# Performance work log

Measured on AMD Instinct MI355X. Metric: run time of the kernel, lower is better.

## Reference

```python
import jax, jax.numpy as jnp
import numpy as np

B, N, D, EPG = 64, 1024, 128, 8192          # graphs, nodes/graph, feat dim, edges/graph
NTOT, ETOT = B * N, B * EPG
RATIO, LAMB, NEG = 0.8, 1.0, 0.2
K = int(np.ceil(RATIO * N))                  # 820 kept nodes per graph (static)


def setup_inputs() -> dict:
    key = jax.random.key(0)
    k1, k2, k3, k4, k5, k6 = jax.random.split(key, 6)
    feat = jax.random.normal(k1, (NTOT, D), jnp.float32)
    offs = (jnp.arange(B, dtype=jnp.int32) * N)[:, None]
    src = (jax.random.randint(k2, (B, EPG), 0, N, jnp.int32) + offs).reshape(-1)
    dst = (jax.random.randint(k3, (B, EPG), 0, N, jnp.int32) + offs).reshape(-1)
    e_feat = jnp.ones((ETOT,), jnp.float32)  # default e_feat=None -> ones
    # xavier-normal-ish params
    W = jax.random.normal(k4, (D, D), jnp.float32) * (2.0 / (D + D)) ** 0.5
    a = jax.random.normal(k5, (D, 1), jnp.float32) * (2.0 / (D + 1)) ** 0.5
    att = jax.random.normal(k6, (1, 2 * D), jnp.float32) * (2.0 / (1 + 2 * D)) ** 0.5
    return {"feat": feat, "e_feat": e_feat, "W": W, "a": a, "att": att,
            "src": src, "dst": dst}


def sparsemax(z, axis):
    """Dense sparsemax along `axis` (shift-invariant, same as edge_sparsemax
    per destination-node group after max subtraction)."""
    n = z.shape[axis]
    zs = -jnp.sort(-z, axis=axis)                      # descending
    cs = jnp.cumsum(zs, axis=axis)
    shp = [1] * z.ndim
    shp[axis] = n
    r = jnp.arange(1, n + 1, dtype=z.dtype).reshape(shp)
    supp = (1.0 + r * zs) > cs
    kz = supp.sum(axis=axis, keepdims=True)            # support size
    tau = (jnp.take_along_axis(cs, kz - 1, axis=axis) - 1.0) / kz.astype(z.dtype)
    return jnp.clip(z - tau, 0.0)


def reference(feat, e_feat, W, a, att, src, dst):
    # ---- NodeInfoScoreLayer (sym_norm=True) ----
    ones_e = jnp.ones_like(e_feat)
    out_deg = jax.ops.segment_sum(ones_e, src, NTOT)   # degrees incl. self loops
    in_deg = jax.ops.segment_sum(ones_e, dst, NTOT)
    sn = jnp.maximum(out_deg, 1.0) ** -0.5
    dn = jnp.maximum(in_deg, 1.0) ** -0.5
    nonself = (src != dst).astype(feat.dtype)          # remove_self_loop
    msg = (feat * sn[:, None])[src] * (e_feat * nonself)[:, None]   # u_mul_e
    agg = jax.ops.segment_sum(msg, dst, NTOT)                        # sum -> h
    info = jnp.abs(feat - agg * dn[:, None]).sum(axis=1)

    # ---- node attention gate ----
    attn = jax.nn.sigmoid(jax.nn.leaky_relu((feat @ W) @ a, 0.2).squeeze(-1))
    x_score = info * attn

    # ---- per-graph top-k (equal graph sizes -> static k) ----
    _, idx = jax.lax.top_k(x_score.reshape(B, N), K)
    perm = (idx + jnp.arange(B, dtype=idx.dtype)[:, None] * N).reshape(-1)
    feat_p = feat[perm]                                # [B*K, D]

    # ---- structure learning, sample=False path: per-graph dense blocks ----
    maskarr = jnp.full((NTOT,), -1, jnp.int32).at[perm].set(
        jnp.arange(B * K, dtype=jnp.int32))
    nr, nc = maskarr[src], maskarr[dst]
    valid = (nr >= 0) & (nc >= 0)                      # edges of pooled subgraph
    nr0 = jnp.where(valid, nr, 0)
    nc0 = jnp.where(valid, nc, 0)
    bb, ii, jj = nr0 // K, nr0 % K, nc0 % K            # block-diagonal coords

    fp = feat_p.reshape(B, K, D)
    wsrc = fp @ att[0, :D]                             # [B, K]
    wdst = fp @ att[0, D:]
    Wblk = jax.nn.leaky_relu(wsrc[:, :, None] + wdst[:, None, :], NEG)  # [B,K,K]
    Wblk = Wblk.at[bb, ii, jj].add(jnp.where(valid, LAMB * e_feat, 0.0))

    # edge_sparsemax: normalize over incoming edges of each dst node
    weights = sparsemax(Wblk, axis=1)                  # over src axis
    weights = jnp.where(jnp.abs(weights) > 1e-9, weights, 0.0)

    return feat_p, weights, perm, x_score
```

## Files before the change

### kernel.cpp

```cpp
#include <hip/hip_runtime.h>
#include <math.h>


static constexpr int B_    = 64;
static constexpr int N_    = 1024;
static constexpr int D_    = 128;
static constexpr int NTOT_ = B_ * N_;
static constexpr int ETOT_ = B_ * 8192;
static constexpr int K_    = 820;
static constexpr int BK_   = B_ * K_;
static constexpr float NEG_ = 0.2f;
static constexpr int CH_   = 128;
static constexpr int CPB_  = 7;
static constexpr int CAP_  = 64;

__device__ __forceinline__ float lrelu(float x) { return x >= 0.f ? x : NEG_ * x; }

__global__ void k_wa(const float* __restrict__ W, const float* __restrict__ a,
                     float* __restrict__ waf) {
  int d = threadIdx.x;
  double s = 0.0;
  for (int k = 0; k < D_; ++k) s += (double)W[d * D_ + k] * (double)a[k];
  waf[d] = (float)s;
}

__global__ void k_deg(const int* __restrict__ src, const int* __restrict__ dst,
                      int* __restrict__ outd, int* __restrict__ ind) {
  int e = blockIdx.x * 256 + threadIdx.x;
  atomicAdd(&outd[src[e]], 1);
  atomicAdd(&ind[dst[e]], 1);
}

__global__ void k_scansum(const int* __restrict__ in, int n, int* __restrict__ bsum) {
  int blk = blockIdx.x, t = threadIdx.x;
  int base = blk * 1024 + t * 4;
  int s = 0;
#pragma unroll
  for (int q = 0; q < 4; ++q) { int i = base + q; if (i < n) s += in[i]; }
#pragma unroll
  for (int off = 32; off > 0; off >>= 1) s += __shfl_down(s, off);
  __shared__ int ws[4];
  int w = t >> 6, lane = t & 63;
  if (lane == 0) ws[w] = s;
  __syncthreads();
  if (t == 0) bsum[blk] = ws[0] + ws[1] + ws[2] + ws[3];
}

__global__ void k_scanout(const int* __restrict__ in, int n,
                          const int* __restrict__ bsum, int* __restrict__ out) {
  int blk = blockIdx.x, t = threadIdx.x;
  int w = t >> 6, lane = t & 63;
  __shared__ int sbase;
  __shared__ int wtot[4];
  if (w == 0) {
    int v = (lane < blk) ? bsum[lane] : 0;
#pragma unroll
    for (int off = 32; off > 0; off >>= 1) v += __shfl_down(v, off);
    if (lane == 0) sbase = v;
  }
  int base = blk * 1024 + t * 4;
  int a0 = (base < n) ? in[base] : 0;
  int a1 = (base + 1 < n) ? in[base + 1] : 0;
  int a2 = (base + 2 < n) ? in[base + 2] : 0;
  int a3 = (base + 3 < n) ? in[base + 3] : 0;
  int s = a0 + a1 + a2 + a3;
  int inc = s;
#pragma unroll
  for (int off = 1; off < 64; off <<= 1) {
    int vv = __shfl_up(inc, off);
    if (lane >= off) inc += vv;
  }
  if (lane == 63) wtot[w] = inc;
  __syncthreads();
  int wbase = 0;
  for (int q = 0; q < w; ++q) wbase += wtot[q];
  int ex = sbase + wbase + inc - s;
  if (base < n) out[base] = ex; ex += a0;
  if (base + 1 < n) out[base + 1] = ex; ex += a1;
  if (base + 2 < n) out[base + 2] = ex; ex += a2;
  if (base + 3 < n) out[base + 3] = ex; ex += a3;
  if (blk == (int)gridDim.x - 1 && t == 255) out[n] = ex;
}

__global__ void k_fillcsr(const int* __restrict__ dst, const int* __restrict__ rowptr,
                          int* __restrict__ cursor, int* __restrict__ col) {
  int e = blockIdx.x * 256 + threadIdx.x;
  int v = dst[e];
  int p = atomicAdd(&cursor[v], 1);
  col[rowptr[v] + p] = e;
}

__global__ void k_agg(const float* __restrict__ feat, const float* __restrict__ e_feat,
                      const int* __restrict__ src, const int* __restrict__ col,
                      const int* __restrict__ rowptr, const int* __restrict__ outd,
                      const int* __restrict__ ind, const float* __restrict__ waf,
                      float* __restrict__ out_xs) {
  __shared__ int su[4][CAP_];
  __shared__ float ssc[4][CAP_];
  int g = blockIdx.x;
  int vb = (g & 7) * 2048 + (g >> 3);
  int w = threadIdx.x >> 6, lane = threadIdx.x & 63;
  int v = vb * 4 + w;
  int r0 = rowptr[v], r1 = rowptr[v + 1];
  int m = r1 - r0;
  int mm = m < CAP_ ? m : CAP_;
  for (int s = lane; s < mm; s += 64) {
    int e = col[r0 + s];
    int u = src[e];
    float sc = (u == v) ? 0.f : e_feat[e] / sqrtf(fmaxf((float)outd[u], 1.f));
    su[w][s] = u;
    ssc[w][s] = sc;
  }
  __syncthreads();
  const float2* f2 = (const float2*)feat;
  float2 f = f2[(size_t)v * 64 + lane];
  float ax = 0.f, ay = 0.f;
  int s = 0;
  for (; s + 4 <= mm; s += 4) {
    int u0 = su[w][s], u1 = su[w][s + 1], u2 = su[w][s + 2], u3 = su[w][s + 3];
    float c0 = ssc[w][s], c1 = ssc[w][s + 1], c2 = ssc[w][s + 2], c3 = ssc[w][s + 3];
    float2 f0 = f2[(size_t)u0 * 64 + lane];
    float2 f1 = f2[(size_t)u1 * 64 + lane];
    float2 fq = f2[(size_t)u2 * 64 + lane];
    float2 f3 = f2[(size_t)u3 * 64 + lane];
    ax += f0.x * c0 + f1.x * c1 + fq.x * c2 + f3.x * c3;
    ay += f0.y * c0 + f1.y * c1 + fq.y * c2 + f3.y * c3;
  }
  for (; s < mm; ++s) {
    float2 fu = f2[(size_t)su[w][s] * 64 + lane];
    ax += fu.x * ssc[w][s];
    ay += fu.y * ssc[w][s];
  }
  for (int sP = r0 + CAP_; sP < r1; ++sP) {
    int e = col[sP];
    int u = src[e];
    if (u == v) continue;
    float sc = e_feat[e] / sqrtf(fmaxf((float)outd[u], 1.f));
    float2 fu = f2[(size_t)u * 64 + lane];
    ax += fu.x * sc;
    ay += fu.y * sc;
  }
  float dn = 1.f / sqrtf(fmaxf((float)ind[v], 1.f));
  float info = fabsf(f.x - ax * dn) + fabsf(f.y - ay * dn);
  float dot = f.x * waf[2 * lane] + f.y * waf[2 * lane + 1];
#pragma unroll
  for (int off = 32; off > 0; off >>= 1) {
    info += __shfl_down(info, off);
    dot  += __shfl_down(dot, off);
  }
  if (lane == 0) {
    float sA = dot >= 0.f ? dot : 0.2f * dot;
    float attn = 1.f / (1.f + expf(-sA));
    out_xs[v] = info * attn;
  }
}

__global__ void k_topk(const float* __restrict__ xs, float* __restrict__ out_perm,
                       int* __restrict__ perm_i, int* __restrict__ maskarr) {
  __shared__ unsigned long long dv[1024];
  int b = blockIdx.x, t = threadIdx.x;
  for (int i = t; i < 1024; i += 512) {
    unsigned bits = __float_as_uint(xs[b * 1024 + i]);
    dv[i] = ((unsigned long long)bits << 32) | (unsigned)(N_ - 1 - i);
  }
  __syncthreads();
  for (int k2 = 2; k2 <= 1024; k2 <<= 1) {
    for (int j = k2 >> 1; j > 0; j >>= 1) {
      for (int i = t; i < 1024; i += 512) {
        int ixj = i ^ j;
        if (ixj > i) {
          unsigned long long a = dv[i], c = dv[ixj];
          bool dir = ((i & k2) == 0);
          if ((a > c) != dir) { dv[i] = c; dv[ixj] = a; }
        }
      }
      __syncthreads();
    }
  }
  for (int r = t; r < K_; r += 512) {
    int idx = N_ - 1 - (int)(dv[r] & 0xFFFFFFFFull);
    int node = b * N_ + idx;
    int pos = b * K_ + r;
    out_perm[pos] = (float)node;
    perm_i[pos] = node;
    maskarr[node] = pos;
  }
}

__global__ void k_gather(const float* __restrict__ feat, const int* __restrict__ perm_i,
                         const float* __restrict__ att, float* __restrict__ out_featp,
                         float* __restrict__ wsrc, float* __restrict__ wdst) {
  int g = blockIdx.x;
  int vb = (g & 7) * 1640 + (g >> 3);
  int gid = vb * 256 + threadIdx.x;
  int p = gid >> 6, lane = gid & 63;
  int node = perm_i[p];
  float2 f = ((const float2*)feat)[(size_t)node * 64 + lane];
  ((float2*)out_featp)[(size_t)p * 64 + lane] = f;
  float s1 = f.x * att[2 * lane] + f.y * att[2 * lane + 1];
  float s2 = f.x * att[D_ + 2 * lane] + f.y * att[D_ + 2 * lane + 1];
#pragma unroll
  for (int off = 32; off > 0; off >>= 1) {
    s1 += __shfl_down(s1, off);
    s2 += __shfl_down(s2, off);
  }
  if (lane == 0) { wsrc[p] = s1; wdst[p] = s2; }
}

__global__ void k_cnt2(const int* __restrict__ src, const int* __restrict__ dst,
                       const int* __restrict__ maskarr, int* __restrict__ cnt2) {
  int e = blockIdx.x * 256 + threadIdx.x;
  int nr = maskarr[src[e]], nc = maskarr[dst[e]];
  if (nr >= 0 && nc >= 0) atomicAdd(&cnt2[nc], 1);
}

__global__ void k_fill2(const int* __restrict__ src, const int* __restrict__ dst,
                        const int* __restrict__ maskarr, const float* __restrict__ e_feat,
                        const int* __restrict__ rowptr2, int* __restrict__ cursor2,
                        int* __restrict__ colii, float* __restrict__ colval) {
  int e = blockIdx.x * 256 + threadIdx.x;
  int nr = maskarr[src[e]], nc = maskarr[dst[e]];
  if (nr >= 0 && nc >= 0) {
    int p = atomicAdd(&cursor2[nc], 1);
    int s = rowptr2[nc] + p;
    colii[s] = nr;
    colval[s] = 1.0f * e_feat[e];
  }
}

__global__ void k_dedupe(const int* __restrict__ rowptr2, int* __restrict__ colii,
                         float* __restrict__ colval, int* __restrict__ ucnt,
                         const float* __restrict__ wsrc, float2* __restrict__ bval) {
  int c = blockIdx.x * 256 + threadIdx.x;
  int r0 = rowptr2[c], r1 = rowptr2[c + 1];
  int w = r0;
  for (int s = r0; s < r1; ++s) {
    int ii = colii[s];
    if (ii < 0) continue;
    float E = colval[s];
    for (int t2 = s + 1; t2 < r1; ++t2)
      if (colii[t2] == ii) { E += colval[t2]; colii[t2] = -1; }
    colii[w] = ii; colval[w] = E; ++w;
  }
  ucnt[c] = w - r0;
  for (int s = r0; s < w; ++s) bval[s] = make_float2(wsrc[colii[s]], colval[s]);
}

__global__ void k_gsort(const float* __restrict__ wsrc, float* __restrict__ ws_sorted,
                        float* __restrict__ psum) {
  __shared__ float sv[1024];
  __shared__ float sc[1024];
  int b = blockIdx.x, t = threadIdx.x;
  for (int i = t; i < 1024; i += 512) sv[i] = (i < K_) ? wsrc[b * K_ + i] : -INFINITY;
  __syncthreads();
  for (int k2 = 2; k2 <= 1024; k2 <<= 1) {
    for (int j = k2 >> 1; j > 0; j >>= 1) {
      for (int i = t; i < 1024; i += 512) {
        int ixj = i ^ j;
        if (ixj > i) {
          float a = sv[i], c = sv[ixj];
          bool dir = ((i & k2) == 0);
          bool swapv = dir ? (c > a) : (a > c);
          if (swapv) { sv[i] = c; sv[ixj] = a; }
        }
      }
      __syncthreads();
    }
  }
  for (int i = t; i < 1024; i += 512) { ws_sorted[b * 1024 + i] = sv[i]; sc[i] = sv[i]; }
  __syncthreads();
  for (int off = 1; off < 1024; off <<= 1) {
    float tmp[2];
    for (int i = t, q = 0; i < 1024; i += 512, ++q) tmp[q] = (i >= off) ? sc[i - off] : 0.f;
    __syncthreads();
    for (int i = t, q = 0; i < 1024; i += 512, ++q) sc[i] += tmp[q];
    __syncthreads();
  }
  if (t == 0) psum[b * 1025] = 0.f;
  for (int i = t; i < 1024; i += 512) psum[b * 1025 + 1 + i] = sc[i];
}

__device__ __forceinline__ int cnt_gt_rng(const float* __restrict__ arr, float thr,
                                          int lo, int hi) {
  while (lo < hi) {
    int mid = (lo + hi) >> 1;
    if (arr[mid] > thr) lo = mid + 1; else hi = mid;
  }
  return lo;
}

__global__ void __launch_bounds__(128) k_tau(
    const float* __restrict__ wdst,
    const float* __restrict__ ws_sorted, const float* __restrict__ psum,
    const int* __restrict__ rowptr2, const int* __restrict__ ucnt,
    const float2* __restrict__ bval, float* __restrict__ tauv) {
  __shared__ float swss[1024];
  __shared__ float sps[1025];
  int b = blockIdx.x / CPB_;
  int chunk = blockIdx.x % CPB_;
  int t0 = threadIdx.x;
  for (int i = t0; i < 1024; i += 128) swss[i] = ws_sorted[b * 1024 + i];
  for (int i = t0; i < 1025; i += 128) sps[i] = psum[b * 1025 + i];
  __syncthreads();

  int j = chunk * CH_ + t0;
  if (j >= K_) return;
  int c = b * K_ + j;

  float wd = wdst[c];
  int p = cnt_gt_rng(swss, -wd, 0, K_);
  float psp = sps[p];
  int r0 = rowptr2[c], m = ucnt[c];

  float mz = lrelu(swss[0] + wd);
  for (int s = 0; s < m; ++s) {
    float2 v = bval[r0 + s];
    mz = fmaxf(mz, lrelu(v.x + wd) + v.y);
  }

  float lo = mz - 1.0f, hi = mz;
  int nmin = 0, nmax = K_;
  for (int it = 0; it < 22; ++it) {
    float t = 0.5f * (lo + hi);
    float wthr = (t >= 0.f ? t : 5.f * t) - wd;
    int n = cnt_gt_rng(swss, wthr, nmin, nmax);
    float bsum = (n <= p) ? (sps[n] + n * wd)
                          : (psp + p * wd + NEG_ * (sps[n] - psp + (n - p) * wd));
    float g = bsum - n * t;
    for (int s = 0; s < m; ++s) {
      float2 v = bval[r0 + s];
      float bse = lrelu(v.x + wd);
      g += fmaxf(bse + v.y - t, 0.f) - fmaxf(bse - t, 0.f);
    }
    if (g > 1.f) { lo = t; nmax = n; } else { hi = t; nmin = n; }
  }
  float t = lo;
  float wthr = (t >= 0.f ? t : 5.f * t) - wd;
  int n = cnt_gt_rng(swss, wthr, nmin, nmax);
  float S = (n <= p) ? (sps[n] + n * wd)
                     : (psp + p * wd + NEG_ * (sps[n] - psp + (n - p) * wd));
  int cc = n;
  for (int s = 0; s < m; ++s) {
    float2 v = bval[r0 + s];
    float bse = lrelu(v.x + wd);
    float zz = bse + v.y;
    if (v.x > wthr) { S -= bse; cc -= 1; }
    if (zz > t)     { S += zz;  cc += 1; }
  }
  float tau = (cc < 1) ? (mz - 1.0f) : ((S - 1.0f) / (float)cc);
  tau = fminf(fmaxf(tau, mz - 1.0f), mz);
  tauv[c] = tau;
}

__global__ void k_dense(const float* __restrict__ wsrc, const float* __restrict__ wdst,
                        const float* __restrict__ tauv, float* __restrict__ out_w) {
  int t = threadIdx.x;
  int j4 = t * 4;
  if (j4 >= K_) return;
  int row = blockIdx.x;
  int b = row / K_;
  const float4* wd4 = (const float4*)(wdst + b * K_);
  const float4* ta4 = (const float4*)(tauv + b * K_);
  float ws = wsrc[row];
  float4 wd = wd4[t];
  float4 ta = ta4[t];
  float4 o;
  float z;
  z = lrelu(ws + wd.x) - ta.x; o.x = (z > 1e-9f) ? z : 0.f;
  z = lrelu(ws + wd.y) - ta.y; o.y = (z > 1e-9f) ? z : 0.f;
  z = lrelu(ws + wd.z) - ta.z; o.z = (z > 1e-9f) ? z : 0.f;
  z = lrelu(ws + wd.w) - ta.w; o.w = (z > 1e-9f) ? z : 0.f;
  ((float4*)(out_w + (size_t)row * K_))[t] = o;
}

__global__ void k_fix(const float* __restrict__ wsrc, const float* __restrict__ wdst,
                      const float* __restrict__ tauv, const int* __restrict__ rowptr2,
                      const int* __restrict__ ucnt, const int* __restrict__ colii,
                      const float* __restrict__ colval, float* __restrict__ out_w) {
  int c = blockIdx.x * 256 + threadIdx.x;
  int b = c / K_;
  int j = c - b * K_;
  float wd = wdst[c], ta = tauv[c];
  int r0 = rowptr2[c], m = ucnt[c];
  for (int s = 0; s < m; ++s) {
    int nr = colii[r0 + s];
    float z = lrelu(wsrc[nr] + wd) + colval[r0 + s];
    float v = z - ta;
    out_w[(size_t)nr * K_ + j] = (v > 1e-9f) ? v : 0.f;
  }
}

extern "C" void kernel_launch(void* const* d_in, const int* in_sizes, int n_in,
                              void* d_out, int out_size, void* d_ws, size_t ws_size,
                              hipStream_t stream) {
  const float* feat   = (const float*)d_in[0];
  const float* e_feat = (const float*)d_in[1];
  const float* W      = (const float*)d_in[2];
  const float* a      = (const float*)d_in[3];
  const float* att    = (const float*)d_in[4];
  const int*   src    = (const int*)d_in[5];
  const int*   dst    = (const int*)d_in[6];

  float* out_featp = (float*)d_out;
  float* out_w     = out_featp + (size_t)BK_ * D_;
  float* out_perm  = out_w + (size_t)BK_ * K_;
  float* out_xs    = out_perm + BK_;

  char* wsp = (char*)d_ws;
  auto carve = [&](size_t bytes) -> void* {
    void* pp = (void*)wsp;
    wsp += (bytes + 255) & ~(size_t)255;
    return pp;
  };
  float* waf       = (float*)carve((size_t)D_ * 4);
  float* wsrc      = (float*)carve((size_t)BK_ * 4);
  float* wdst      = (float*)carve((size_t)BK_ * 4);
  float* tauv      = (float*)carve((size_t)BK_ * 4);
  float* colval    = (float*)carve((size_t)ETOT_ * 4);
  float2* bval     = (float2*)carve((size_t)ETOT_ * 8);
  float* ws_sorted = (float*)carve((size_t)B_ * 1024 * 4);
  float* psum      = (float*)carve((size_t)B_ * 1025 * 4);
  int* rowptr      = (int*)carve((size_t)(NTOT_ + 1) * 4);
  int* rowptr2     = (int*)carve((size_t)(BK_ + 1) * 4);
  int* col         = (int*)carve((size_t)ETOT_ * 4);
  int* colii       = (int*)carve((size_t)ETOT_ * 4);
  int* perm_i      = (int*)carve((size_t)BK_ * 4);
  int* bsumA       = (int*)carve(64 * 4);
  int* bsumB       = (int*)carve(64 * 4);
  size_t zbytes    = ((size_t)NTOT_ * 3 + (size_t)BK_ * 2) * 4;
  int* zblk        = (int*)carve(zbytes);
  int* in_deg      = zblk;
  int* out_deg     = zblk + NTOT_;
  int* cursor      = zblk + 2 * NTOT_;
  int* cnt2        = zblk + 3 * NTOT_;
  int* cursor2     = cnt2 + BK_;
  int* maskarr     = (int*)carve((size_t)NTOT_ * 4);

  hipMemsetAsync(zblk, 0, zbytes, stream);
  hipMemsetAsync(maskarr, 0xFF, (size_t)NTOT_ * 4, stream);

  const int nbA = (NTOT_ + 1023) / 1024;
  const int nbB = (BK_ + 1023) / 1024;

  k_wa<<<1, 128, 0, stream>>>(W, a, waf);
  k_deg<<<ETOT_ / 256, 256, 0, stream>>>(src, dst, out_deg, in_deg);
  k_scansum<<<nbA, 256, 0, stream>>>(in_deg, NTOT_, bsumA);
  k_scanout<<<nbA, 256, 0, stream>>>(in_deg, NTOT_, bsumA, rowptr);
  k_fillcsr<<<ETOT_ / 256, 256, 0, stream>>>(dst, rowptr, cursor, col);
  k_agg<<<NTOT_ / 4, 256, 0, stream>>>(feat, e_feat, src, col, rowptr, out_deg, in_deg,
                                       waf, out_xs);
  k_topk<<<B_, 512, 0, stream>>>(out_xs, out_perm, perm_i, maskarr);
  k_gather<<<BK_ / 4, 256, 0, stream>>>(feat, perm_i, att, out_featp, wsrc, wdst);
  k_cnt2<<<ETOT_ / 256, 256, 0, stream>>>(src, dst, maskarr, cnt2);
  k_scansum<<<nbB, 256, 0, stream>>>(cnt2, BK_, bsumB);
  k_scanout<<<nbB, 256, 0, stream>>>(cnt2, BK_, bsumB, rowptr2);
  k_fill2<<<ETOT_ / 256, 256, 0, stream>>>(src, dst, maskarr, e_feat, rowptr2, cursor2,
                                           colii, colval);
  k_dedupe<<<BK_ / 256, 256, 0, stream>>>(rowptr2, colii, colval, cursor2, wsrc, bval);
  k_gsort<<<B_, 512, 0, stream>>>(wsrc, ws_sorted, psum);
  k_tau<<<B_ * CPB_, 128, 0, stream>>>(wdst, ws_sorted, psum, rowptr2, cursor2,
                                       bval, tauv);
  k_dense<<<BK_, 256, 0, stream>>>(wsrc, wdst, tauv, out_w);
  k_fix<<<BK_ / 256, 256, 0, stream>>>(wsrc, wdst, tauv, rowptr2, cursor2, colii, colval,
                                       out_w);
}
```

Baseline: 544.0 us.

## Fuse small kernels, use single-pass lookback scans, and widen dense writes

Merges the W·a kernel into the degree kernel and the gather into the pooled-edge count. It fuses the second scan with the per-graph sort, folds dedupe into the tau kernel, and replaces two-pass scans with single-pass scans that spin on flagged partial sums. The dense weight writer now emits four rows per block with nontemporal stores. The aim is to cut launch count and extra passes over memory for the large K×K output. The spin-wait scan depends on all earlier blocks being co-resident or scheduled first, which is a risk if they are not.

```diff
diff --git a/kernel.cpp b/kernel.cpp
--- a/kernel.cpp
+++ b/kernel.cpp
@@ -13,52 +13,46 @@
 static constexpr int CH_   = 128;
 static constexpr int CPB_  = 7;
 static constexpr int CAP_  = 64;
+static constexpr int NSA_  = (NTOT_ + 2047) / 2048;
+static constexpr int NSB_  = (BK_ + 2047) / 2048;
+static constexpr int SFLAG = 0x40000000;
+
+typedef float fvec4 __attribute__((ext_vector_type(4)));
 
 __device__ __forceinline__ float lrelu(float x) { return x >= 0.f ? x : NEG_ * x; }
 
-__global__ void k_wa(const float* __restrict__ W, const float* __restrict__ a,
-                     float* __restrict__ waf) {
-  int d = threadIdx.x;
-  double s = 0.0;
-  for (int k = 0; k < D_; ++k) s += (double)W[d * D_ + k] * (double)a[k];
-  waf[d] = (float)s;
-}
-
-__global__ void k_deg(const int* __restrict__ src, const int* __restrict__ dst,
-                      int* __restrict__ outd, int* __restrict__ ind) {
-  int e = blockIdx.x * 256 + threadIdx.x;
-  atomicAdd(&outd[src[e]], 1);
-  atomicAdd(&ind[dst[e]], 1);
-}
-
-__global__ void k_scansum(const int* __restrict__ in, int n, int* __restrict__ bsum) {
-  int blk = blockIdx.x, t = threadIdx.x;
-  int base = blk * 1024 + t * 4;
-  int s = 0;
-#pragma unroll
-  for (int q = 0; q < 4; ++q) { int i = base + q; if (i < n) s += in[i]; }
-#pragma unroll
-  for (int off = 32; off > 0; off >>= 1) s += __shfl_down(s, off);
-  __shared__ int ws[4];
+__global__ void k_deg_wa(const int* __restrict__ src, const int* __restrict__ dst,
+                         int* __restrict__ outd, int* __restrict__ ind,
+                         const float* __restrict__ W, const float* __restrict__ a,
+                         float* __restrict__ waf) {
+  int blk = blockIdx.x;
+  if (blk < ETOT_ / 256) {
+    int e = blk * 256 + threadIdx.x;
+    atomicAdd(&outd[src[e]], 1);
+    atomicAdd(&ind[dst[e]], 1);
+  } else {
+    int q = blk - ETOT_ / 256;
+    int w = threadIdx.x >> 6, lane = threadIdx.x & 63;
+    int wid = q * 4 + w;
+    double a0 = (double)a[2 * lane], a1 = (double)a[2 * lane + 1];
+#pragma unroll
+    for (int r = 0; r < 4; ++r) {
+      int d = wid * 4 + r;
+      double s = (double)W[d * D_ + 2 * lane] * a0
+               + (double)W[d * D_ + 2 * lane + 1] * a1;
+#pragma unroll
+      for (int off = 32; off > 0; off >>= 1) s += __shfl_down(s, off);
+      if (lane == 0) waf[d] = (float)s;
+    }
+  }
+}
+
+__device__ __forceinline__ void scan2048(const int* __restrict__ in, int n, int blk,
+                                         int nblk, int* __restrict__ partials,
+                                         int* __restrict__ out) {
+  int t = threadIdx.x;
   int w = t >> 6, lane = t & 63;
-  if (lane == 0) ws[w] = s;
-  __syncthreads();
-  if (t == 0) bsum[blk] = ws[0] + ws[1] + ws[2] + ws[3];
-}
-
-__global__ void k_scanout(const int* __restrict__ in, int n,
-                          const int* __restrict__ bsum, int* __restrict__ out) {
-  int blk = blockIdx.x, t = threadIdx.x;
-  int w = t >> 6, lane = t & 63;
-  __shared__ int sbase;
-  __shared__ int wtot[4];
-  if (w == 0) {
-    int v = (lane < blk) ? bsum[lane] : 0;
-#pragma unroll
-    for (int off = 32; off > 0; off >>= 1) v += __shfl_down(v, off);
-    if (lane == 0) sbase = v;
-  }
-  int base = blk * 1024 + t * 4;
+  int base = blk * 2048 + t * 4;
   int a0 = (base < n) ? in[base] : 0;
   int a1 = (base + 1 < n) ? in[base + 1] : 0;
   int a2 = (base + 2 < n) ? in[base + 2] : 0;
@@ -67,19 +61,47 @@
   int inc = s;
 #pragma unroll
   for (int off = 1; off < 64; off <<= 1) {
-    int vv = __shfl_up(inc, off);
-    if (lane >= off) inc += vv;
-  }
+    int v = __shfl_up(inc, off);
+    if (lane >= off) inc += v;
+  }
+  __shared__ int wtot[8];
+  __shared__ int sbase;
   if (lane == 63) wtot[w] = inc;
   __syncthreads();
+  if (t == 0) {
+    int btot = 0;
+#pragma unroll
+    for (int q2 = 0; q2 < 8; ++q2) btot += wtot[q2];
+    __hip_atomic_store(&partials[blk], btot | SFLAG, __ATOMIC_RELEASE,
+                       __HIP_MEMORY_SCOPE_AGENT);
+  }
+  if (t < 64) {
+    int v = 0;
+    if (t < blk) {
+      do {
+        v = __hip_atomic_load(&partials[t], __ATOMIC_ACQUIRE,
+                              __HIP_MEMORY_SCOPE_AGENT);
+      } while (!(v & SFLAG));
+      v &= ~SFLAG;
+    }
+#pragma unroll
+    for (int off = 32; off > 0; off >>= 1) v += __shfl_down(v, off);
+    if (t == 0) sbase = v;
+  }
+  __syncthreads();
   int wbase = 0;
-  for (int q = 0; q < w; ++q) wbase += wtot[q];
+  for (int q2 = 0; q2 < w; ++q2) wbase += wtot[q2];
   int ex = sbase + wbase + inc - s;
   if (base < n) out[base] = ex; ex += a0;
   if (base + 1 < n) out[base + 1] = ex; ex += a1;
   if (base + 2 < n) out[base + 2] = ex; ex += a2;
   if (base + 3 < n) out[base + 3] = ex; ex += a3;
-  if (blk == (int)gridDim.x - 1 && t == 255) out[n] = ex;
+  if (blk == nblk - 1 && t == 511) out[n] = ex;
+}
+
+__global__ void k_scanA(const int* __restrict__ in, int* __restrict__ partials,
+                        int* __restrict__ out) {
+  scan2048(in, NTOT_, blockIdx.x, NSA_, partials, out);
 }
 
 __global__ void k_fillcsr(const int* __restrict__ dst, const int* __restrict__ rowptr,
@@ -187,70 +209,44 @@
   }
 }
 
-__global__ void k_gather(const float* __restrict__ feat, const int* __restrict__ perm_i,
-                         const float* __restrict__ att, float* __restrict__ out_featp,
-                         float* __restrict__ wsrc, float* __restrict__ wdst) {
-  int g = blockIdx.x;
-  int vb = (g & 7) * 1640 + (g >> 3);
-  int gid = vb * 256 + threadIdx.x;
-  int p = gid >> 6, lane = gid & 63;
-  int node = perm_i[p];
-  float2 f = ((const float2*)feat)[(size_t)node * 64 + lane];
-  ((float2*)out_featp)[(size_t)p * 64 + lane] = f;
-  float s1 = f.x * att[2 * lane] + f.y * att[2 * lane + 1];
-  float s2 = f.x * att[D_ + 2 * lane] + f.y * att[D_ + 2 * lane + 1];
-#pragma unroll
-  for (int off = 32; off > 0; off >>= 1) {
-    s1 += __shfl_down(s1, off);
-    s2 += __shfl_down(s2, off);
-  }
-  if (lane == 0) { wsrc[p] = s1; wdst[p] = s2; }
-}
-
-__global__ void k_cnt2(const int* __restrict__ src, const int* __restrict__ dst,
-                       const int* __restrict__ maskarr, int* __restrict__ cnt2) {
-  int e = blockIdx.x * 256 + threadIdx.x;
-  int nr = maskarr[src[e]], nc = maskarr[dst[e]];
-  if (nr >= 0 && nc >= 0) atomicAdd(&cnt2[nc], 1);
-}
-
-__global__ void k_fill2(const int* __restrict__ src, const int* __restrict__ dst,
-                        const int* __restrict__ maskarr, const float* __restrict__ e_feat,
-                        const int* __restrict__ rowptr2, int* __restrict__ cursor2,
-                        int* __restrict__ colii, float* __restrict__ colval) {
-  int e = blockIdx.x * 256 + threadIdx.x;
-  int nr = maskarr[src[e]], nc = maskarr[dst[e]];
-  if (nr >= 0 && nc >= 0) {
-    int p = atomicAdd(&cursor2[nc], 1);
-    int s = rowptr2[nc] + p;
-    colii[s] = nr;
-    colval[s] = 1.0f * e_feat[e];
-  }
-}
-
-__global__ void k_dedupe(const int* __restrict__ rowptr2, int* __restrict__ colii,
-                         float* __restrict__ colval, int* __restrict__ ucnt,
-                         const float* __restrict__ wsrc, float2* __restrict__ bval) {
-  int c = blockIdx.x * 256 + threadIdx.x;
-  int r0 = rowptr2[c], r1 = rowptr2[c + 1];
-  int w = r0;
-  for (int s = r0; s < r1; ++s) {
-    int ii = colii[s];
-    if (ii < 0) continue;
-    float E = colval[s];
-    for (int t2 = s + 1; t2 < r1; ++t2)
-      if (colii[t2] == ii) { E += colval[t2]; colii[t2] = -1; }
-    colii[w] = ii; colval[w] = E; ++w;
-  }
-  ucnt[c] = w - r0;
-  for (int s = r0; s < w; ++s) bval[s] = make_float2(wsrc[colii[s]], colval[s]);
-}
-
-__global__ void k_gsort(const float* __restrict__ wsrc, float* __restrict__ ws_sorted,
-                        float* __restrict__ psum) {
+__global__ void k_gather_cnt2(const float* __restrict__ feat, const int* __restrict__ perm_i,
+                              const float* __restrict__ att, float* __restrict__ out_featp,
+                              float* __restrict__ wsrc, float* __restrict__ wdst,
+                              const int* __restrict__ src, const int* __restrict__ dst,
+                              const int* __restrict__ maskarr, int* __restrict__ cnt2) {
+  int blk = blockIdx.x;
+  if (blk < BK_ / 4) {
+    int vb = (blk & 7) * 1640 + (blk >> 3);
+    int gid = vb * 256 + threadIdx.x;
+    int p = gid >> 6, lane = gid & 63;
+    int node = perm_i[p];
+    float2 f = ((const float2*)feat)[(size_t)node * 64 + lane];
+    ((float2*)out_featp)[(size_t)p * 64 + lane] = f;
+    float s1 = f.x * att[2 * lane] + f.y * att[2 * lane + 1];
+    float s2 = f.x * att[D_ + 2 * lane] + f.y * att[D_ + 2 * lane + 1];
+#pragma unroll
+    for (int off = 32; off > 0; off >>= 1) {
+      s1 += __shfl_down(s1, off);
+      s2 += __shfl_down(s2, off);
+    }
+    if (lane == 0) { wsrc[p] = s1; wdst[p] = s2; }
+  } else {
+    int e = (blk - BK_ / 4) * 256 + threadIdx.x;
+    int nr = maskarr[src[e]], nc = maskarr[dst[e]];
+    if (nr >= 0 && nc >= 0) atomicAdd(&cnt2[nc], 1);
+  }
+}
+
+__global__ void k_scanB_gsort(const int* __restrict__ cnt2, int* __restrict__ partials,
+                              int* __restrict__ rowptr2, const float* __restrict__ wsrc,
+                              float* __restrict__ ws_sorted, float* __restrict__ psum) {
+  if (blockIdx.x < NSB_) {
+    scan2048(cnt2, BK_, blockIdx.x, NSB_, partials, rowptr2);
+    return;
+  }
   __shared__ float sv[1024];
   __shared__ float sc[1024];
-  int b = blockIdx.x, t = threadIdx.x;
+  int b = blockIdx.x - NSB_, t = threadIdx.x;
   for (int i = t; i < 1024; i += 512) sv[i] = (i < K_) ? wsrc[b * K_ + i] : -INFINITY;
   __syncthreads();
   for (int k2 = 2; k2 <= 1024; k2 <<= 1) {
@@ -280,6 +276,20 @@
   for (int i = t; i < 1024; i += 512) psum[b * 1025 + 1 + i] = sc[i];
 }
 
+__global__ void k_fill2(const int* __restrict__ src, const int* __restrict__ dst,
+                        const int* __restrict__ maskarr, const float* __restrict__ e_feat,
+                        const int* __restrict__ rowptr2, int* __restrict__ cursor2,
+                        int* __restrict__ colii, float* __restrict__ colval) {
+  int e = blockIdx.x * 256 + threadIdx.x;
+  int nr = maskarr[src[e]], nc = maskarr[dst[e]];
+  if (nr >= 0 && nc >= 0) {
+    int p = atomicAdd(&cursor2[nc], 1);
+    int s = rowptr2[nc] + p;
+    colii[s] = nr;
+    colval[s] = 1.0f * e_feat[e];
+  }
+}
+
 __device__ __forceinline__ int cnt_gt_rng(const float* __restrict__ arr, float thr,
                                           int lo, int hi) {
   while (lo < hi) {
@@ -292,8 +302,10 @@
 __global__ void __launch_bounds__(128) k_tau(
     const float* __restrict__ wdst,
     const float* __restrict__ ws_sorted, const float* __restrict__ psum,
-    const int* __restrict__ rowptr2, const int* __restrict__ ucnt,
-    const float2* __restrict__ bval, float* __restrict__ tauv) {
+    const int* __restrict__ rowptr2, int* __restrict__ ucnt,
+    int* __restrict__ colii, float* __restrict__ colval,
+    const float* __restrict__ wsrc, float2* __restrict__ bval,
+    float* __restrict__ tauv) {
   __shared__ float swss[1024];
   __shared__ float sps[1025];
   int b = blockIdx.x / CPB_;
@@ -307,10 +319,23 @@
   if (j >= K_) return;
   int c = b * K_ + j;
 
+  int r0 = rowptr2[c], r1 = rowptr2[c + 1];
+  int wp = r0;
+  for (int s = r0; s < r1; ++s) {
+    int ii = colii[s];
+    if (ii < 0) continue;
+    float E = colval[s];
+    for (int t2 = s + 1; t2 < r1; ++t2)
+      if (colii[t2] == ii) { E += colval[t2]; colii[t2] = -1; }
+    colii[wp] = ii; colval[wp] = E; ++wp;
+  }
+  int m = wp - r0;
+  ucnt[c] = m;
+  for (int s = r0; s < wp; ++s) bval[s] = make_float2(wsrc[colii[s]], colval[s]);
+
   float wd = wdst[c];
   int p = cnt_gt_rng(swss, -wd, 0, K_);
   float psp = sps[p];
-  int r0 = rowptr2[c], m = ucnt[c];
 
   float mz = lrelu(swss[0] + wd);
   for (int s = 0; s < m; ++s) {
@@ -352,25 +377,28 @@
   tauv[c] = tau;
 }
 
-__global__ void k_dense(const float* __restrict__ wsrc, const float* __restrict__ wdst,
-                        const float* __restrict__ tauv, float* __restrict__ out_w) {
+__global__ void k_dense4(const float* __restrict__ wsrc, const float* __restrict__ wdst,
+                         const float* __restrict__ tauv, float* __restrict__ out_w) {
   int t = threadIdx.x;
   int j4 = t * 4;
   if (j4 >= K_) return;
-  int row = blockIdx.x;
-  int b = row / K_;
-  const float4* wd4 = (const float4*)(wdst + b * K_);
-  const float4* ta4 = (const float4*)(tauv + b * K_);
-  float ws = wsrc[row];
-  float4 wd = wd4[t];
-  float4 ta = ta4[t];
-  float4 o;
-  float z;
-  z = lrelu(ws + wd.x) - ta.x; o.x = (z > 1e-9f) ? z : 0.f;
-  z = lrelu(ws + wd.y) - ta.y; o.y = (z > 1e-9f) ? z : 0.f;
-  z = lrelu(ws + wd.z) - ta.z; o.z = (z > 1e-9f) ? z : 0.f;
-  z = lrelu(ws + wd.w) - ta.w; o.w = (z > 1e-9f) ? z : 0.f;
-  ((float4*)(out_w + (size_t)row * K_))[t] = o;
+  int r0 = blockIdx.x * 4;
+  int b = r0 / K_;
+  float4 wd = ((const float4*)(wdst + b * K_))[t];
+  float4 ta = ((const float4*)(tauv + b * K_))[t];
+  float4 ws4 = ((const float4*)wsrc)[blockIdx.x];
+  const float wss[4] = {ws4.x, ws4.y, ws4.z, ws4.w};
+#pragma unroll
+  for (int q = 0; q < 4; ++q) {
+    float ws = wss[q];
+    fvec4 o;
+    float z;
+    z = lrelu(ws + wd.x) - ta.x; o.x = (z > 1e-9f) ? z : 0.f;
+    z = lrelu(ws + wd.y) - ta.y; o.y = (z > 1e-9f) ? z : 0.f;
+    z = lrelu(ws + wd.z) - ta.z; o.z = (z > 1e-9f) ? z : 0.f;
+    z = lrelu(ws + wd.w) - ta.w; o.w = (z > 1e-9f) ? z : 0.f;
+    __builtin_nontemporal_store(o, ((fvec4*)(out_w + (size_t)(r0 + q) * K_)) + t);
+  }
 }
 
 __global__ void k_fix(const float* __restrict__ wsrc, const float* __restrict__ wdst,
@@ -425,42 +453,35 @@
   int* col         = (int*)carve((size_t)ETOT_ * 4);
   int* colii       = (int*)carve((size_t)ETOT_ * 4);
   int* perm_i      = (int*)carve((size_t)BK_ * 4);
-  int* bsumA       = (int*)carve(64 * 4);
-  int* bsumB       = (int*)carve(64 * 4);
-  size_t zbytes    = ((size_t)NTOT_ * 3 + (size_t)BK_ * 2) * 4;
+  size_t zbytes    = ((size_t)NTOT_ * 3 + (size_t)BK_ * 2 + 64) * 4;
   int* zblk        = (int*)carve(zbytes);
   int* in_deg      = zblk;
   int* out_deg     = zblk + NTOT_;
   int* cursor      = zblk + 2 * NTOT_;
   int* cnt2        = zblk + 3 * NTOT_;
   int* cursor2     = cnt2 + BK_;
+  int* partA       = cursor2 + BK_;
+  int* partB       = partA + 32;
   int* maskarr     = (int*)carve((size_t)NTOT_ * 4);
 
   hipMemsetAsync(zblk, 0, zbytes, stream);
   hipMemsetAsync(maskarr, 0xFF, (size_t)NTOT_ * 4, stream);
 
-  const int nbA = (NTOT_ + 1023) / 1024;
-  const int nbB = (BK_ + 1023) / 1024;
-
-  k_wa<<<1, 128, 0, stream>>>(W, a, waf);
-  k_deg<<<ETOT_ / 256, 256, 0, stream>>>(src, dst, out_deg, in_deg);
-  k_scansum<<<nbA, 256, 0, stream>>>(in_deg, NTOT_, bsumA);
-  k_scanout<<<nbA, 256, 0, stream>>>(in_deg, NTOT_, bsumA, rowptr);
+  k_deg_wa<<<ETOT_ / 256 + 8, 256, 0, stream>>>(src, dst, out_deg, in_deg, W, a, waf);
+  k_scanA<<<NSA_, 512, 0, stream>>>(in_deg, partA, rowptr);
   k_fillcsr<<<ETOT_ / 256, 256, 0, stream>>>(dst, rowptr, cursor, col);
   k_agg<<<NTOT_ / 4, 256, 0, stream>>>(feat, e_feat, src, col, rowptr, out_deg, in_deg,
                                        waf, out_xs);
   k_topk<<<B_, 512, 0, stream>>>(out_xs, out_perm, perm_i, maskarr);
-  k_gather<<<BK_ / 4, 256, 0, stream>>>(feat, perm_i, att, out_featp, wsrc, wdst);
-  k_cnt2<<<ETOT_ / 256, 256, 0, stream>>>(src, dst, maskarr, cnt2);
-  k_scansum<<<nbB, 256, 0, stream>>>(cnt2, BK_, bsumB);
-  k_scanout<<<nbB, 256, 0, stream>>>(cnt2, BK_, bsumB, rowptr2);
+  k_gather_cnt2<<<BK_ / 4 + ETOT_ / 256, 256, 0, stream>>>(
+      feat, perm_i, att, out_featp, wsrc, wdst, src, dst, maskarr, cnt2);
+  k_scanB_gsort<<<NSB_ + B_, 512, 0, stream>>>(cnt2, partB, rowptr2, wsrc,
+                                               ws_sorted, psum);
   k_fill2<<<ETOT_ / 256, 256, 0, stream>>>(src, dst, maskarr, e_feat, rowptr2, cursor2,
                                            colii, colval);
-  k_dedupe<<<BK_ / 256, 256, 0, stream>>>(rowptr2, colii, colval, cursor2, wsrc, bval);
-  k_gsort<<<B_, 512, 0, stream>>>(wsrc, ws_sorted, psum);
   k_tau<<<B_ * CPB_, 128, 0, stream>>>(wdst, ws_sorted, psum, rowptr2, cursor2,
-                                       bval, tauv);
-  k_dense<<<BK_, 256, 0, stream>>>(wsrc, wdst, tauv, out_w);
+                                       colii, colval, wsrc, bval, tauv);
+  k_dense4<<<BK_ / 4, 256, 0, stream>>>(wsrc, wdst, tauv, out_w);
   k_fix<<<BK_ / 256, 256, 0, stream>>>(wsrc, wdst, tauv, rowptr2, cursor2, colii, colval,
                                        out_w);
 }
```

Measured after the change: 539.8 us. No clear change (-0.8%).
